# Optimization experiments

Measured on AMD Instinct MI355X. Metric: run time of the kernel, lower is better.

Reference implementation:

```python
import jax, jax.numpy as jnp
import numpy as np

HEAD_DIM = 64
AGGR = 4  # attn_aggr_ratio
BN_EPS = 1e-5


def _conv1x1(x, W, b=None):
    # x: [N, Cin, L], W: [Cout, Cin] -> [N, Cout, L]
    y = jnp.einsum('ncl,oc->nol', x, W)
    if b is not None:
        y = y + b[None, :, None]
    return y


def _bn(x, gamma, beta, mean, var):
    # BatchNorm1d, eval mode (running stats). x: [N, C, L]
    inv = gamma * jax.lax.rsqrt(var + BN_EPS)
    return x * inv[None, :, None] + (beta - mean * inv)[None, :, None]


def setup_inputs() -> dict:
    key = jax.random.key(0)
    ks = jax.random.split(key, 8)
    N, C, L = 4, 256, 4096
    s = 1.0 / np.sqrt(C)
    inp = {
        'x': jax.random.normal(ks[0], (N, C, L), jnp.float32),
        'Wq': jax.random.normal(ks[1], (C, C), jnp.float32) * s,
        'bq': jnp.zeros((C,), jnp.float32),
        'Wk': jax.random.normal(ks[2], (C, C), jnp.float32) * s,
        'bk': jnp.zeros((C,), jnp.float32),
        'Wv': jax.random.normal(ks[3], (C, C), jnp.float32) * s,
        'bv': jnp.zeros((C,), jnp.float32),
        'Wo': jax.random.normal(ks[4], (C, C), jnp.float32) * s,
        'bo': jnp.zeros((C,), jnp.float32),
        'Wa': jax.random.normal(ks[5], (C, C), jnp.float32) * s,
        'g1': jnp.ones((C,), jnp.float32), 'b1': jnp.zeros((C,), jnp.float32),
        'm1': jnp.zeros((C,), jnp.float32), 'v1': jnp.ones((C,), jnp.float32),
        'g2': jnp.ones((C,), jnp.float32), 'b2': jnp.zeros((C,), jnp.float32),
        'm2': jnp.zeros((C,), jnp.float32), 'v2': jnp.ones((C,), jnp.float32),
    }
    return inp


def reference(x, Wq, bq, Wk, bk, Wv, bv, Wo, bo, Wa,
              g1, b1, m1, v1, g2, b2, m2, v2):
    N, C, L = x.shape
    H, E = C // HEAD_DIM, HEAD_DIM
    # q projection on full-resolution input
    q = _conv1x1(x, Wq, bq).reshape(N, H, E, L)
    # LocalAwareAggregationBlock: avg+max pool (kernel=AGGR, L divisible), 1x1 conv, BN
    xp = x.reshape(N, C, L // AGGR, AGGR)
    xa = xp.mean(axis=-1) + xp.max(axis=-1)          # [N, C, L//AGGR]
    xa = _conv1x1(xa, Wa)                             # bias=False
    xa = _bn(xa, g1, b1, m1, v1)
    # post-aggregation norm
    xa = _bn(xa, g2, b2, m2, v2)
    k = _conv1x1(xa, Wk, bk).reshape(N, H, E, -1)     # [N, H, E, L2]
    v = _conv1x1(xa, Wv, bv).reshape(N, H, E, -1)
    # attention: softmax((q/sqrt(E))^T k) @ v^T
    scale = 1.0 / np.sqrt(E)
    scores = jnp.einsum('nhel,nhem->nhlm', q * scale, k)  # [N, H, L, L2]
    attn = jax.nn.softmax(scores, axis=-1)
    o = jnp.einsum('nhlm,nhem->nhel', attn, v).reshape(N, C, L)
    return _conv1x1(o, Wo, bo)
```

## Files before the change

### kernel.cpp

```cpp
#include <hip/hip_runtime.h>
#include <stdint.h>

constexpr int NBATCH = 4;
constexpr int CH     = 256;
constexpr int LEN    = 4096;
constexpr int LPOOL  = 1024;
constexpr int NH     = 4;
constexpr int HD     = 64;

typedef __attribute__((ext_vector_type(8))) short short8;
typedef __attribute__((ext_vector_type(4))) float float4e;

__device__ __forceinline__ unsigned short f2bf(float f) {
    union { unsigned int i; float f; } v; v.f = f;
    unsigned int lsb = (v.i >> 16) & 1u;
    v.i += 0x7fffu + lsb;
    return (unsigned short)(v.i >> 16);
}
__device__ __forceinline__ unsigned pack2bf(float lo, float hi) {
    unsigned a = __float_as_uint(lo) + 0x8000u;
    unsigned b = __float_as_uint(hi) + 0x8000u;
    return __builtin_amdgcn_perm(b, a, 0x07060302u);
}

__global__ __launch_bounds__(256) void setup_kernel(
    const float* __restrict__ w0, const float* __restrict__ w1,
    const float* __restrict__ w2, const float* __restrict__ w3,
    const float* __restrict__ w4, unsigned short* __restrict__ outW,
    const float* __restrict__ g1, const float* __restrict__ b1,
    const float* __restrict__ m1, const float* __restrict__ v1,
    const float* __restrict__ g2, const float* __restrict__ b2,
    const float* __restrict__ m2, const float* __restrict__ v2,
    float* __restrict__ scale, float* __restrict__ shift,
    const float* __restrict__ bk, const float* __restrict__ bv,
    float* __restrict__ bkv)
{
    int b = blockIdx.x, t = threadIdx.x;
    if (b < 320) {
        int gid = b * 256 + t;
        int w = gid >> 14;
        int off = (gid & 16383) * 4;
        const float* src = (w == 0) ? w0 : (w == 1) ? w1 : (w == 2) ? w2 : (w == 3) ? w3 : w4;
        float4 v = *(const float4*)(src + off);
        uint2 pk;
        pk.x = pack2bf(v.x, v.y);
        pk.y = pack2bf(v.z, v.w);
        *(uint2*)(outW + w * 65536 + off) = pk;
    } else {
        float inv1 = g1[t] * rsqrtf(v1[t] + 1e-5f);
        float inv2 = g2[t] * rsqrtf(v2[t] + 1e-5f);
        scale[t] = inv1 * inv2;
        shift[t] = (b1[t] - m1[t] * inv1) * inv2 + (b2[t] - m2[t] * inv2);
        bkv[t] = bk[t];
        bkv[256 + t] = bv[t];
    }
}

__global__ __launch_bounds__(256) void transpool(
    const float* __restrict__ x, unsigned short* __restrict__ xbf,
    unsigned short* __restrict__ poolT)
{
    __shared__ float T[64][65];
    __shared__ float P16[64][17];
    int n = blockIdx.z, c0 = blockIdx.y * 64, l0 = blockIdx.x * 64;
    const float* xp = x + ((size_t)n * CH + c0) * LEN + l0;
    int t = threadIdx.x;
    #pragma unroll
    for (int i = 0; i < 4; i++) {
        int idx = t + i * 256;
        int c = idx >> 4, l4 = idx & 15;
        float4 v = *(const float4*)(xp + (size_t)c * LEN + l4 * 4);
        T[c][l4 * 4 + 0] = v.x; T[c][l4 * 4 + 1] = v.y;
        T[c][l4 * 4 + 2] = v.z; T[c][l4 * 4 + 3] = v.w;
        P16[c][l4] = (v.x + v.y + v.z + v.w) * 0.25f
                   + fmaxf(fmaxf(v.x, v.y), fmaxf(v.z, v.w));
    }
    __syncthreads();
    unsigned short* op = xbf + ((size_t)n * LEN + l0) * CH + c0;
    #pragma unroll
    for (int i = 0; i < 4; i++) {
        int idx = t + i * 256;
        int l = idx >> 4, c4 = idx & 15;
        uint2 pk;
        pk.x = pack2bf(T[c4 * 4 + 0][l], T[c4 * 4 + 1][l]);
        pk.y = pack2bf(T[c4 * 4 + 2][l], T[c4 * 4 + 3][l]);
        *(uint2*)(op + (size_t)l * CH + c4 * 4) = pk;
    }
    int p0 = l0 >> 2;
    #pragma unroll
    for (int k = 0; k < 2; k++) {
        int p = (t >> 5) + k * 8;
        int c2 = (t & 31) * 2;
        unsigned pk = pack2bf(P16[c2][p], P16[c2 + 1][p]);
        *(unsigned*)(poolT + ((size_t)n * LPOOL + p0 + p) * CH + c0 + c2) = pk;
    }
}

__global__ __launch_bounds__(256) void gemm_mfma(
    const unsigned short* __restrict__ A,
    const unsigned short* __restrict__ B, size_t bBatch,
    const float* __restrict__ biasRow,
    const float* __restrict__ scale, const float* __restrict__ shift,
    float* __restrict__ outF, size_t oFBatch,
    unsigned short* __restrict__ out1, size_t o1Batch, int cs1,
    unsigned short* __restrict__ out2, size_t o2Batch, int rs2, int rowSplit,
    int NN, float outScale)
{
    __shared__ unsigned short smem[2 * 128 * 72];
    unsigned short* As = smem;
    unsigned short* Bs = smem + 128 * 72;

    int n = blockIdx.z;
    int t = threadIdx.x;
    int wave = t >> 6, lane = t & 63, m = lane & 15, quad = lane >> 4;
    int wm = wave & 1, wn = wave >> 1;
    int rowTile = blockIdx.y * 128;
    int col0 = blockIdx.x * 128;

    const unsigned short* Ab = A + (size_t)rowTile * 256;
    const unsigned short* Bb = B + (size_t)n * bBatch + (size_t)col0 * 256;

    float4e acc[4][4] = {};

    for (int kk = 0; kk < 256; kk += 64) {
        #pragma unroll
        for (int i = 0; i < 4; i++) {
            int idx = t + i * 256;
            int row = idx >> 3, ch = idx & 7;
            *(uint4*)&As[row * 72 + ch * 8] = *(const uint4*)(Ab + (size_t)row * 256 + kk + ch * 8);
            *(uint4*)&Bs[row * 72 + ch * 8] = *(const uint4*)(Bb + (size_t)row * 256 + kk + ch * 8);
        }
        __syncthreads();
        #pragma unroll
        for (int kc = 0; kc < 2; kc++) {
            short8 af[4], bfr[4];
            #pragma unroll
            for (int i = 0; i < 4; i++)
                af[i] = *(const short8*)&As[(wm * 64 + i * 16 + m) * 72 + kc * 32 + quad * 8];
            #pragma unroll
            for (int j = 0; j < 4; j++)
                bfr[j] = *(const short8*)&Bs[(wn * 64 + j * 16 + m) * 72 + kc * 32 + quad * 8];
            #pragma unroll
            for (int i = 0; i < 4; i++)
                #pragma unroll
                for (int j = 0; j < 4; j++)
                    acc[i][j] = __builtin_amdgcn_mfma_f32_16x16x32_bf16(af[i], bfr[j], acc[i][j], 0, 0, 0);
        }
        __syncthreads();
    }

    if (outF) {
        float* TOf = (float*)smem;
        float* dst = outF + (size_t)n * oFBatch;
        #pragma unroll
        for (int half = 0; half < 2; half++) {
            __syncthreads();
            if (wm == half) {
                #pragma unroll
                for (int i = 0; i < 4; i++) {
                    int rowL = i * 16 + quad * 4;
                    int rowG = rowTile + half * 64 + rowL;
                    float br[4], sc[4], sh[4];
                    #pragma unroll
                    for (int r = 0; r < 4; r++) {
                        br[r] = biasRow ? biasRow[rowG + r] : 0.0f;
                        sc[r] = scale ? scale[rowG + r] : 1.0f;
                        sh[r] = shift ? shift[rowG + r] : 0.0f;
                    }
                    #pragma unroll
                    for (int j = 0; j < 4; j++) {
                        int colL = wn * 64 + j * 16 + m;
                        float4e c = acc[i][j];
                        #pragma unroll
                        for (int r = 0; r < 4; r++)
                            TOf[(rowL + r) * 128 + colL] = ((c[r] + br[r]) * sc[r] + sh[r]) * outScale;
                    }
                }
            }
            __syncthreads();
            #pragma unroll
            for (int w = 0; w < 8; w++) {
                int idx = t + w * 256;
                int row = idx >> 5, c4 = idx & 31;
                *(float4*)(dst + (size_t)(rowTile + half * 64 + row) * NN + col0 + c4 * 4) =
                    *(const float4*)&TOf[row * 128 + c4 * 4];
            }
        }
        return;
    }

    bool mode2 = (rowTile >= rowSplit);
    unsigned short* TO = smem;
    #pragma unroll
    for (int i = 0; i < 4; i++) {
        int rowL = wm * 64 + i * 16 + quad * 4;
        int rowG = rowTile + rowL;
        float br[4], sc[4], sh[4];
        #pragma unroll
        for (int r = 0; r < 4; r++) {
            br[r] = biasRow ? biasRow[rowG + r] : 0.0f;
            sc[r] = scale ? scale[rowG + r] : 1.0f;
            sh[r] = shift ? shift[rowG + r] : 0.0f;
        }
        #pragma unroll
        for (int j = 0; j < 4; j++) {
            int colL = wn * 64 + j * 16 + m;
            float4e c = acc[i][j];
            float v0 = ((c[0] + br[0]) * sc[0] + sh[0]) * outScale;
            float v1 = ((c[1] + br[1]) * sc[1] + sh[1]) * outScale;
            float v2 = ((c[2] + br[2]) * sc[2] + sh[2]) * outScale;
            float v3 = ((c[3] + br[3]) * sc[3] + sh[3]) * outScale;
            if (!mode2) {
                uint2 pk;
                pk.x = pack2bf(v0, v1);
                pk.y = pack2bf(v2, v3);
                *(uint2*)&TO[colL * 136 + rowL] = pk;
            } else {
                TO[(rowL + 0) * 136 + colL] = f2bf(v0);
                TO[(rowL + 1) * 136 + colL] = f2bf(v1);
                TO[(rowL + 2) * 136 + colL] = f2bf(v2);
                TO[(rowL + 3) * 136 + colL] = f2bf(v3);
            }
        }
    }
    __syncthreads();
    if (!mode2) {
        unsigned short* dst = out1 + (size_t)n * o1Batch;
        #pragma unroll
        for (int w = 0; w < 8; w++) {
            int idx = t + w * 256;
            int l = idx >> 4, ch = idx & 15;
            *(uint4*)(dst + (size_t)(col0 + l) * cs1 + rowTile + ch * 8) =
                *(const uint4*)&TO[l * 136 + ch * 8];
        }
    } else {
        unsigned short* dst = out2 + (size_t)n * o2Batch;
        int rowBase = rowTile - rowSplit;
        #pragma unroll
        for (int w = 0; w < 8; w++) {
            int idx = t + w * 256;
            int row = idx >> 4, ch = idx & 15;
            *(uint4*)(dst + (size_t)(rowBase + row) * rs2 + col0 + ch * 8) =
                *(const uint4*)&TO[row * 136 + ch * 8];
        }
    }
}

__global__ __launch_bounds__(256) void attn_mfma(
    const unsigned short* __restrict__ Qb,
    const unsigned short* __restrict__ Kb,
    const unsigned short* __restrict__ Vb,
    unsigned short* __restrict__ Obf)
{
    __shared__ unsigned short Ks[128 * 72];
    __shared__ unsigned short Vs[64 * 136];
    __shared__ unsigned short Ps[4 * 32 * 136];

    int qb = blockIdx.x;
    int h  = blockIdx.y;
    int n  = blockIdx.z;
    int t  = threadIdx.x;
    int wave = t >> 6, lane = t & 63;
    int m = lane & 15, quad = lane >> 4;
    int l0 = qb * 128 + wave * 32;

    const unsigned short* qp = Qb + ((size_t)n * LEN + l0 + m) * CH + h * HD + quad * 8;
    short8 bQ[2][2];
    bQ[0][0] = *(const short8*)qp;
    bQ[0][1] = *(const short8*)(qp + 32);
    bQ[1][0] = *(const short8*)(qp + 16 * CH);
    bQ[1][1] = *(const short8*)(qp + 16 * CH + 32);

    float4e Oa[2][4] = {};
    float l_run[2] = {0.0f, 0.0f};
    unsigned short* Pw = Ps + wave * 32 * 136;

    const unsigned short* KgBase = Kb + (size_t)n * LPOOL * CH + h * HD;
    const unsigned short* VgBase = Vb + ((size_t)n * CH + h * HD) * LPOOL;
    const float NEG = -17.312340f;

    for (int kt = 0; kt < 8; kt++) {
        __syncthreads();
        {
            const unsigned short* Kg = KgBase + (size_t)kt * 128 * CH;
            #pragma unroll
            for (int i = 0; i < 4; i++) {
                int idx = t + i * 256;
                int row = idx >> 3, ch = idx & 7;
                *(uint4*)&Ks[row * 72 + ch * 8] = *(const uint4*)(Kg + (size_t)row * CH + ch * 8);
            }
        }
        {
            const unsigned short* Vg = VgBase + kt * 128;
            #pragma unroll
            for (int i = 0; i < 4; i++) {
                int idx = t + i * 256;
                int e = idx >> 4, ch = idx & 15;
                *(uint4*)&Vs[e * 136 + ch * 8] = *(const uint4*)(Vg + (size_t)e * LPOOL + ch * 8);
            }
        }
        __syncthreads();

        #pragma unroll
        for (int kb = 0; kb < 8; kb++) {
            const unsigned short* kp = &Ks[(kb * 16 + m) * 72 + quad * 8];
            short8 a0 = *(const short8*)kp;
            short8 a1 = *(const short8*)(kp + 32);
            #pragma unroll
            for (int qf = 0; qf < 2; qf++) {
                float4e c = {NEG, NEG, NEG, NEG};
                c = __builtin_amdgcn_mfma_f32_16x16x32_bf16(a0, bQ[qf][0], c, 0, 0, 0);
                c = __builtin_amdgcn_mfma_f32_16x16x32_bf16(a1, bQ[qf][1], c, 0, 0, 0);
                float p0 = exp2f(c[0]);
                float p1 = exp2f(c[1]);
                float p2 = exp2f(c[2]);
                float p3 = exp2f(c[3]);
                l_run[qf] += (p0 + p1) + (p2 + p3);
                uint2 pk;
                pk.x = pack2bf(p0, p1);
                pk.y = pack2bf(p2, p3);
                *(uint2*)&Pw[(qf * 16 + m) * 136 + kb * 16 + quad * 4] = pk;
            }
        }

        #pragma unroll
        for (int ch2 = 0; ch2 < 4; ch2++) {
            short8 bP0 = *(const short8*)&Pw[m * 136 + ch2 * 32 + quad * 8];
            short8 bP1 = *(const short8*)&Pw[(16 + m) * 136 + ch2 * 32 + quad * 8];
            #pragma unroll
            for (int eb = 0; eb < 4; eb++) {
                short8 aV = *(const short8*)&Vs[(eb * 16 + m) * 136 + ch2 * 32 + quad * 8];
                Oa[0][eb] = __builtin_amdgcn_mfma_f32_16x16x32_bf16(aV, bP0, Oa[0][eb], 0, 0, 0);
                Oa[1][eb] = __builtin_amdgcn_mfma_f32_16x16x32_bf16(aV, bP1, Oa[1][eb], 0, 0, 0);
            }
        }
    }

    #pragma unroll
    for (int qf = 0; qf < 2; qf++) {
        float l = l_run[qf];
        l += __shfl_xor(l, 16);
        l += __shfl_xor(l, 32);
        float inv = 1.0f / l;
        unsigned short* op = Obf + ((size_t)n * LEN + l0 + qf * 16 + m) * CH + h * HD;
        #pragma unroll
        for (int eb = 0; eb < 4; eb++) {
            uint2 pk;
            pk.x = pack2bf(Oa[qf][eb][0] * inv, Oa[qf][eb][1] * inv);
            pk.y = pack2bf(Oa[qf][eb][2] * inv, Oa[qf][eb][3] * inv);
            *(uint2*)(op + eb * 16 + quad * 4) = pk;
        }
    }
}

extern "C" void kernel_launch(void* const* d_in, const int* in_sizes, int n_in,
                              void* d_out, int out_size, void* d_ws, size_t ws_size,
                              hipStream_t stream)
{
    const float* x  = (const float*)d_in[0];
    const float* Wq = (const float*)d_in[1];
    const float* bq = (const float*)d_in[2];
    const float* Wk = (const float*)d_in[3];
    const float* bk = (const float*)d_in[4];
    const float* Wv = (const float*)d_in[5];
    const float* bv = (const float*)d_in[6];
    const float* Wo = (const float*)d_in[7];
    const float* bo = (const float*)d_in[8];
    const float* Wa = (const float*)d_in[9];
    const float* g1 = (const float*)d_in[10];
    const float* b1 = (const float*)d_in[11];
    const float* m1 = (const float*)d_in[12];
    const float* v1 = (const float*)d_in[13];
    const float* g2 = (const float*)d_in[14];
    const float* b2 = (const float*)d_in[15];
    const float* m2 = (const float*)d_in[16];
    const float* v2 = (const float*)d_in[17];

    float* wsf      = (float*)d_ws;
    float* bn_scale = wsf;
    float* bn_shift = wsf + 256;
    float* bkv      = wsf + 512;
    unsigned short* Wbf   = (unsigned short*)(wsf + 1024);
    unsigned short* xbf   = Wbf + 5 * 65536;
    unsigned short* poolT = xbf   + (size_t)NBATCH * LEN * CH;
    unsigned short* xabf  = poolT + (size_t)NBATCH * LPOOL * CH;
    unsigned short* Kbf   = xabf  + (size_t)NBATCH * LPOOL * CH;
    unsigned short* Vbf   = Kbf   + (size_t)NBATCH * LPOOL * CH;
    unsigned short* Qbf   = Vbf   + (size_t)NBATCH * LPOOL * CH;
    unsigned short* Obf   = Qbf   + (size_t)NBATCH * LEN * CH;

    setup_kernel<<<321, 256, 0, stream>>>(Wq, Wk, Wv, Wo, Wa, Wbf,
        g1, b1, m1, v1, g2, b2, m2, v2, bn_scale, bn_shift, bk, bv, bkv);

    transpool<<<dim3(64, 4, 4), 256, 0, stream>>>(x, xbf, poolT);

    gemm_mfma<<<dim3(32, 2, 4), 256, 0, stream>>>(
        Wbf + 0 * 65536, xbf, (size_t)LEN * CH, bq, nullptr, nullptr,
        nullptr, 0, Qbf, (size_t)LEN * CH, 256, nullptr, 0, 0, 1 << 30,
        LEN, 0.18033688f);

    gemm_mfma<<<dim3(8, 2, 4), 256, 0, stream>>>(
        Wbf + 4 * 65536, poolT, (size_t)LPOOL * CH, nullptr, bn_scale, bn_shift,
        nullptr, 0, xabf, (size_t)LPOOL * CH, 256, nullptr, 0, 0, 1 << 30,
        LPOOL, 1.0f);

    gemm_mfma<<<dim3(8, 4, 4), 256, 0, stream>>>(
        Wbf + 1 * 65536, xabf, (size_t)LPOOL * CH, bkv, nullptr, nullptr,
        nullptr, 0, Kbf, (size_t)LPOOL * CH, 256, Vbf, (size_t)LPOOL * CH, LPOOL, 256,
        LPOOL, 1.0f);

    attn_mfma<<<dim3(LEN / 128, NH, NBATCH), 256, 0, stream>>>(Qbf, Kbf, Vbf, Obf);

    gemm_mfma<<<dim3(32, 2, 4), 256, 0, stream>>>(
        Wbf + 3 * 65536, Obf, (size_t)LEN * CH, bo, nullptr, nullptr,
        (float*)d_out, (size_t)CH * LEN, nullptr, 0, 0, nullptr, 0, 0, 1 << 30,
        LEN, 1.0f);
}
```

Before: 180.4 us.

## Merge setup into transpool, register-prefetch K/V, pass P via lane shuffles

Folds the weight-conversion/BN setup kernel into the transpose-pool kernel as extra blocks, removing one launch. In the attention kernel, the next K/V tile is prefetched into registers while the current tile is computed, overlapping global loads with MFMA work. The probability tile P is now handed from the score MFMA layout to the PV MFMA operand layout with cross-lane shuffles instead of a round trip through shared memory, which removes the Ps buffer and its LDS traffic. The cost is higher register pressure from the prefetch registers and extra shuffle instructions.

```diff
diff --git a/kernel.cpp b/kernel.cpp
--- a/kernel.cpp
+++ b/kernel.cpp
@@ -23,7 +23,9 @@
     return __builtin_amdgcn_perm(b, a, 0x07060302u);
 }
 
-__global__ __launch_bounds__(256) void setup_kernel(
+__global__ __launch_bounds__(256) void transpool_setup(
+    const float* __restrict__ x, unsigned short* __restrict__ xbf,
+    unsigned short* __restrict__ poolT,
     const float* __restrict__ w0, const float* __restrict__ w1,
     const float* __restrict__ w2, const float* __restrict__ w3,
     const float* __restrict__ w4, unsigned short* __restrict__ outW,
@@ -35,36 +37,33 @@
     const float* __restrict__ bk, const float* __restrict__ bv,
     float* __restrict__ bkv)
 {
-    int b = blockIdx.x, t = threadIdx.x;
-    if (b < 320) {
-        int gid = b * 256 + t;
-        int w = gid >> 14;
-        int off = (gid & 16383) * 4;
-        const float* src = (w == 0) ? w0 : (w == 1) ? w1 : (w == 2) ? w2 : (w == 3) ? w3 : w4;
-        float4 v = *(const float4*)(src + off);
-        uint2 pk;
-        pk.x = pack2bf(v.x, v.y);
-        pk.y = pack2bf(v.z, v.w);
-        *(uint2*)(outW + w * 65536 + off) = pk;
-    } else {
-        float inv1 = g1[t] * rsqrtf(v1[t] + 1e-5f);
-        float inv2 = g2[t] * rsqrtf(v2[t] + 1e-5f);
-        scale[t] = inv1 * inv2;
-        shift[t] = (b1[t] - m1[t] * inv1) * inv2 + (b2[t] - m2[t] * inv2);
-        bkv[t] = bk[t];
-        bkv[256 + t] = bv[t];
-    }
-}
-
-__global__ __launch_bounds__(256) void transpool(
-    const float* __restrict__ x, unsigned short* __restrict__ xbf,
-    unsigned short* __restrict__ poolT)
-{
     __shared__ float T[64][65];
     __shared__ float P16[64][17];
-    int n = blockIdx.z, c0 = blockIdx.y * 64, l0 = blockIdx.x * 64;
+    int b = blockIdx.x, t = threadIdx.x;
+    if (b >= 1024) {
+        int sb = b - 1024;
+        if (sb < 320) {
+            int gid = sb * 256 + t;
+            int w = gid >> 14;
+            int off = (gid & 16383) * 4;
+            const float* src = (w == 0) ? w0 : (w == 1) ? w1 : (w == 2) ? w2 : (w == 3) ? w3 : w4;
+            float4 v = *(const float4*)(src + off);
+            uint2 pk;
+            pk.x = pack2bf(v.x, v.y);
+            pk.y = pack2bf(v.z, v.w);
+            *(uint2*)(outW + w * 65536 + off) = pk;
+        } else {
+            float inv1 = g1[t] * rsqrtf(v1[t] + 1e-5f);
+            float inv2 = g2[t] * rsqrtf(v2[t] + 1e-5f);
+            scale[t] = inv1 * inv2;
+            shift[t] = (b1[t] - m1[t] * inv1) * inv2 + (b2[t] - m2[t] * inv2);
+            bkv[t] = bk[t];
+            bkv[256 + t] = bv[t];
+        }
+        return;
+    }
+    int n = b >> 8, c0 = ((b >> 6) & 3) * 64, l0 = (b & 63) * 64;
     const float* xp = x + ((size_t)n * CH + c0) * LEN + l0;
-    int t = threadIdx.x;
     #pragma unroll
     for (int i = 0; i < 4; i++) {
         int idx = t + i * 256;
@@ -254,7 +253,6 @@
 {
     __shared__ unsigned short Ks[128 * 72];
     __shared__ unsigned short Vs[64 * 136];
-    __shared__ unsigned short Ps[4 * 32 * 136];
 
     int qb = blockIdx.x;
     int h  = blockIdx.y;
@@ -273,65 +271,83 @@
 
     float4e Oa[2][4] = {};
     float l_run[2] = {0.0f, 0.0f};
-    unsigned short* Pw = Ps + wave * 32 * 136;
 
     const unsigned short* KgBase = Kb + (size_t)n * LPOOL * CH + h * HD;
     const unsigned short* VgBase = Vb + ((size_t)n * CH + h * HD) * LPOOL;
     const float NEG = -17.312340f;
 
+    uint4 kreg[4], vreg[4];
+    #pragma unroll
+    for (int i = 0; i < 4; i++) {
+        int idx = t + i * 256;
+        kreg[i] = *(const uint4*)(KgBase + (size_t)(idx >> 3) * CH + (idx & 7) * 8);
+        vreg[i] = *(const uint4*)(VgBase + (size_t)(idx >> 4) * LPOOL + (idx & 15) * 8);
+    }
+
+    int srcA = ((quad & 1) << 5) + m;
+    int srcB = srcA + 16;
+    bool hiq = quad >= 2;
+
     for (int kt = 0; kt < 8; kt++) {
         __syncthreads();
-        {
-            const unsigned short* Kg = KgBase + (size_t)kt * 128 * CH;
+        #pragma unroll
+        for (int i = 0; i < 4; i++) {
+            int idx = t + i * 256;
+            *(uint4*)&Ks[(idx >> 3) * 72 + (idx & 7) * 8] = kreg[i];
+            *(uint4*)&Vs[(idx >> 4) * 136 + (idx & 15) * 8] = vreg[i];
+        }
+        __syncthreads();
+        if (kt < 7) {
+            const unsigned short* Kg2 = KgBase + (size_t)(kt + 1) * 128 * CH;
+            const unsigned short* Vg2 = VgBase + (kt + 1) * 128;
             #pragma unroll
             for (int i = 0; i < 4; i++) {
                 int idx = t + i * 256;
-                int row = idx >> 3, ch = idx & 7;
-                *(uint4*)&Ks[row * 72 + ch * 8] = *(const uint4*)(Kg + (size_t)row * CH + ch * 8);
+                kreg[i] = *(const uint4*)(Kg2 + (size_t)(idx >> 3) * CH + (idx & 7) * 8);
+                vreg[i] = *(const uint4*)(Vg2 + (size_t)(idx >> 4) * LPOOL + (idx & 15) * 8);
             }
         }
-        {
-            const unsigned short* Vg = VgBase + kt * 128;
-            #pragma unroll
-            for (int i = 0; i < 4; i++) {
-                int idx = t + i * 256;
-                int e = idx >> 4, ch = idx & 15;
-                *(uint4*)&Vs[e * 136 + ch * 8] = *(const uint4*)(Vg + (size_t)e * LPOOL + ch * 8);
-            }
-        }
-        __syncthreads();
-
-        #pragma unroll
-        for (int kb = 0; kb < 8; kb++) {
-            const unsigned short* kp = &Ks[(kb * 16 + m) * 72 + quad * 8];
-            short8 a0 = *(const short8*)kp;
-            short8 a1 = *(const short8*)(kp + 32);
+
+        #pragma unroll
+        for (int ch2 = 0; ch2 < 4; ch2++) {
+            const unsigned short* kpE = &Ks[(ch2 * 32 + m) * 72 + quad * 8];
+            const unsigned short* kpO = &Ks[(ch2 * 32 + 16 + m) * 72 + quad * 8];
+            short8 aE0 = *(const short8*)kpE;
+            short8 aE1 = *(const short8*)(kpE + 32);
+            short8 aO0 = *(const short8*)kpO;
+            short8 aO1 = *(const short8*)(kpO + 32);
+            short8 aV[4];
+            #pragma unroll
+            for (int eb = 0; eb < 4; eb++)
+                aV[eb] = *(const short8*)&Vs[(eb * 16 + m) * 136 + ch2 * 32 + quad * 8];
+
             #pragma unroll
             for (int qf = 0; qf < 2; qf++) {
-                float4e c = {NEG, NEG, NEG, NEG};
-                c = __builtin_amdgcn_mfma_f32_16x16x32_bf16(a0, bQ[qf][0], c, 0, 0, 0);
-                c = __builtin_amdgcn_mfma_f32_16x16x32_bf16(a1, bQ[qf][1], c, 0, 0, 0);
-                float p0 = exp2f(c[0]);
-                float p1 = exp2f(c[1]);
-                float p2 = exp2f(c[2]);
-                float p3 = exp2f(c[3]);
-                l_run[qf] += (p0 + p1) + (p2 + p3);
-                uint2 pk;
-                pk.x = pack2bf(p0, p1);
-                pk.y = pack2bf(p2, p3);
-                *(uint2*)&Pw[(qf * 16 + m) * 136 + kb * 16 + quad * 4] = pk;
-            }
-        }
-
-        #pragma unroll
-        for (int ch2 = 0; ch2 < 4; ch2++) {
-            short8 bP0 = *(const short8*)&Pw[m * 136 + ch2 * 32 + quad * 8];
-            short8 bP1 = *(const short8*)&Pw[(16 + m) * 136 + ch2 * 32 + quad * 8];
-            #pragma unroll
-            for (int eb = 0; eb < 4; eb++) {
-                short8 aV = *(const short8*)&Vs[(eb * 16 + m) * 136 + ch2 * 32 + quad * 8];
-                Oa[0][eb] = __builtin_amdgcn_mfma_f32_16x16x32_bf16(aV, bP0, Oa[0][eb], 0, 0, 0);
-                Oa[1][eb] = __builtin_amdgcn_mfma_f32_16x16x32_bf16(aV, bP1, Oa[1][eb], 0, 0, 0);
+                float4e cE = {NEG, NEG, NEG, NEG};
+                cE = __builtin_amdgcn_mfma_f32_16x16x32_bf16(aE0, bQ[qf][0], cE, 0, 0, 0);
+                cE = __builtin_amdgcn_mfma_f32_16x16x32_bf16(aE1, bQ[qf][1], cE, 0, 0, 0);
+                float4e cO = {NEG, NEG, NEG, NEG};
+                cO = __builtin_amdgcn_mfma_f32_16x16x32_bf16(aO0, bQ[qf][0], cO, 0, 0, 0);
+                cO = __builtin_amdgcn_mfma_f32_16x16x32_bf16(aO1, bQ[qf][1], cO, 0, 0, 0);
+                float pE0 = exp2f(cE[0]), pE1 = exp2f(cE[1]);
+                float pE2 = exp2f(cE[2]), pE3 = exp2f(cE[3]);
+                float pO0 = exp2f(cO[0]), pO1 = exp2f(cO[1]);
+                float pO2 = exp2f(cO[2]), pO3 = exp2f(cO[3]);
+                l_run[qf] += ((pE0 + pE1) + (pE2 + pE3)) + ((pO0 + pO1) + (pO2 + pO3));
+                unsigned ex = pack2bf(pE0, pE1), ey = pack2bf(pE2, pE3);
+                unsigned ox = pack2bf(pO0, pO1), oy = pack2bf(pO2, pO3);
+                unsigned eA0 = __shfl((int)ex, srcA), eA1 = __shfl((int)ey, srcA);
+                unsigned eB0 = __shfl((int)ex, srcB), eB1 = __shfl((int)ey, srcB);
+                unsigned oA0 = __shfl((int)ox, srcA), oA1 = __shfl((int)oy, srcA);
+                unsigned oB0 = __shfl((int)ox, srcB), oB1 = __shfl((int)oy, srcB);
+                union { unsigned u[4]; short8 s; } bP;
+                bP.u[0] = hiq ? oA0 : eA0;
+                bP.u[1] = hiq ? oA1 : eA1;
+                bP.u[2] = hiq ? oB0 : eB0;
+                bP.u[3] = hiq ? oB1 : eB1;
+                #pragma unroll
+                for (int eb = 0; eb < 4; eb++)
+                    Oa[qf][eb] = __builtin_amdgcn_mfma_f32_16x16x32_bf16(aV[eb], bP.s, Oa[qf][eb], 0, 0, 0);
             }
         }
     }
@@ -389,10 +405,9 @@
     unsigned short* Qbf   = Vbf   + (size_t)NBATCH * LPOOL * CH;
     unsigned short* Obf   = Qbf   + (size_t)NBATCH * LEN * CH;
 
-    setup_kernel<<<321, 256, 0, stream>>>(Wq, Wk, Wv, Wo, Wa, Wbf,
+    transpool_setup<<<1345, 256, 0, stream>>>(x, xbf, poolT,
+        Wq, Wk, Wv, Wo, Wa, Wbf,
         g1, b1, m1, v1, g2, b2, m2, v2, bn_scale, bn_shift, bk, bv, bkv);
-
-    transpool<<<dim3(64, 4, 4), 256, 0, stream>>>(x, xbf, poolT);
 
     gemm_mfma<<<dim3(32, 2, 4), 256, 0, stream>>>(
         Wbf + 0 * 65536, xbf, (size_t)LEN * CH, bq, nullptr, nullptr,
```

Measured after the change: 198.0 us. 1.1x slower.
